# Kernel optimization log

Hardware: AMD Instinct MI355X
Metric: run time of the kernel (lower is better)

## Reference

```python
import jax, jax.numpy as jnp
import numpy as np

B, A, F = 8192, 8, 256      # batch, n_agents, per-agent obs feature dim
NA = 16                     # n_actions per agent
H1, H2 = 1024, 1024
OBS_D = A * F               # 2048 flattened obs dim
ACT_D = A * NA              # 128 joint action dim
IN_D = OBS_D + ACT_D        # 2176 MLP input dim


def setup_inputs() -> dict:
    key = jax.random.key(0)
    ks = jax.random.split(key, 8)
    s = 0.02
    return {
        "obs": jax.random.normal(ks[0], (B, A, F), dtype=jnp.float32),
        "all_actions": jax.random.uniform(ks[1], (B, ACT_D), dtype=jnp.float32),
        # per-agent stacked MLP params (agent axis first)
        "W1": jax.random.normal(ks[2], (A, IN_D, H1), dtype=jnp.float32) * s,
        "b1": jnp.zeros((A, H1), dtype=jnp.float32),
        "W2": jax.random.normal(ks[3], (A, H1, H2), dtype=jnp.float32) * s,
        "b2": jnp.zeros((A, H2), dtype=jnp.float32),
        "W3": jax.random.normal(ks[4], (A, H2, NA), dtype=jnp.float32) * s,
        "b3": jnp.zeros((A, NA), dtype=jnp.float32),
    }


def reference(obs, all_actions, W1, b1, W2, b2, W3, b3):
    b_s = obs.shape[0]
    obs_flat = obs.reshape(b_s, OBS_D)                      # [B, A*F]
    # mask[a, g] = 0 on agent a's own action block, 1 elsewhere
    mask = 1.0 - jnp.repeat(jnp.eye(A, dtype=obs.dtype), NA, axis=1)  # [A, A*NA]
    # split W1 into obs / action columns (equivalent to concat-then-dense)
    W1o = W1[:, :OBS_D, :]                                  # [A, OBS_D, H1]
    W1a = W1[:, OBS_D:, :]                                  # [A, ACT_D, H1]
    h1 = jax.nn.relu(
        jnp.einsum("bd,adh->bah", obs_flat, W1o)
        + jnp.einsum("bg,ag,agh->bah", all_actions, mask, W1a)
        + b1
    )                                                        # [B, A, H1]
    h2 = jax.nn.relu(jnp.einsum("bah,ahk->bak", h1, W2) + b2)  # [B, A, H2]
    out = jnp.einsum("bak,akn->ban", h2, W3) + b3              # [B, A, NA]
    return out.reshape(b_s, A * NA)
```

## Files before the change

### kernel.cpp

```cpp
#include <hip/hip_runtime.h>
#include <hip/hip_bf16.h>
#include <cstdint>
#include <cstddef>

typedef __bf16 bf16;
typedef __attribute__((ext_vector_type(8))) __bf16 bf16x8;
typedef __attribute__((ext_vector_type(4))) float f32x4;
typedef __attribute__((ext_vector_type(4))) int i32x4;
typedef __attribute__((address_space(3))) const bf16* lds_cp;

#define B_SZ  8192
#define NAGENT 8
#define NA_N  16
#define OBS_DD 2048
#define ACT_DD 128
#define IN_DD 2176
#define H1_D  1024
#define H2_D  1024

#define BM 256
#define BN 256
#define BK 64
#define GRID_M (B_SZ / BM)
#define GRID_N (1024 / BN)

__device__ __forceinline__ void gload16(const void* g, void* l) {
    __builtin_amdgcn_global_load_lds(
        (__attribute__((address_space(1))) void*)(g),
        (__attribute__((address_space(3))) void*)(l), 16, 0, 0);
}

__global__ void k_prep(const float* __restrict__ obs, const float* __restrict__ act,
                       bf16* __restrict__ xb, const float* __restrict__ b3,
                       float* __restrict__ out, const float* __restrict__ W3,
                       bf16* __restrict__ w3t) {
    const int NX = B_SZ * (IN_DD / 8);
    const int NO = B_SZ * 128 / 4;
    const int NW3 = NAGENT * NA_N * H2_D;
    int idx = blockIdx.x * blockDim.x + threadIdx.x;
    if (idx < NX) {
        const int chunks = IN_DD / 8;
        int b = idx / chunks;
        int c8 = idx - b * chunks;
        const float* src = (c8 < OBS_DD / 8)
            ? (obs + (size_t)b * OBS_DD + c8 * 8)
            : (act + (size_t)b * ACT_DD + (c8 - OBS_DD / 8) * 8);
        float4 v0 = ((const float4*)src)[0];
        float4 v1 = ((const float4*)src)[1];
        bf16x8 o;
        o[0] = (bf16)v0.x; o[1] = (bf16)v0.y; o[2] = (bf16)v0.z; o[3] = (bf16)v0.w;
        o[4] = (bf16)v1.x; o[5] = (bf16)v1.y; o[6] = (bf16)v1.z; o[7] = (bf16)v1.w;
        ((bf16x8*)(xb + (size_t)b * IN_DD))[c8] = o;
    } else if (idx < NX + NO) {
        int i = idx - NX;
        int c = (i & 31) * 4;
        float4 v = make_float4(b3[c], b3[c + 1], b3[c + 2], b3[c + 3]);
        ((float4*)out)[i] = v;
    } else if (idx < NX + NO + NW3) {
        int i = idx - NX - NO;
        int a = i / (NA_N * H2_D);
        int n = (i / H2_D) % NA_N;
        int k = i % H2_D;
        w3t[i] = (bf16)W3[(size_t)a * H2_D * NA_N + (size_t)k * NA_N + n];
    }
}

__global__ void k_transpose_w12(const float* __restrict__ W1, bf16* __restrict__ W1T,
                                const float* __restrict__ W2, bf16* __restrict__ W2T) {
    __shared__ float tile[32][33];
    const int z = blockIdx.z;
    const bool isW1 = (z < 8);
    const int a = isW1 ? z : z - 8;
    const int K = isW1 ? IN_DD : H1_D;
    const int H = 1024;
    const int maskStart = isW1 ? OBS_DD : (1 << 30);
    if (!isW1 && blockIdx.x >= (H1_D / 32)) return;
    const float* s = (isW1 ? W1 : W2) + (size_t)a * K * H;
    bf16* d = (isW1 ? W1T : W2T) + (size_t)a * K * H;
    int k0 = blockIdx.x * 32, h0 = blockIdx.y * 32;
    int tx = threadIdx.x, ty = threadIdx.y;
    #pragma unroll
    for (int i = 0; i < 32; i += 8) {
        int k = k0 + ty + i;
        float v = s[(size_t)k * H + h0 + tx];
        if (k >= maskStart) {
            int g = k - maskStart;
            if ((g >> 4) == a) v = 0.f;
        }
        tile[ty + i][tx] = v;
    }
    __syncthreads();
    #pragma unroll
    for (int i = 0; i < 32; i += 8) {
        d[(size_t)(h0 + ty + i) * K + k0 + tx] = (bf16)tile[tx][ty + i];
    }
}

#define DSR4(d0, d1, d2, d3, addr, O0, O1, O2, O3)                      \
    asm volatile("ds_read_b128 %0, %4 offset:" #O0 "\n\t"               \
                 "ds_read_b128 %1, %4 offset:" #O1 "\n\t"               \
                 "ds_read_b128 %2, %4 offset:" #O2 "\n\t"               \
                 "ds_read_b128 %3, %4 offset:" #O3                      \
                 : "=&v"(d0), "=&v"(d1), "=&v"(d2), "=&v"(d3)           \
                 : "v"(addr))
#define DSR2(d0, d1, addr, O0, O1)                                      \
    asm volatile("ds_read_b128 %0, %2 offset:" #O0 "\n\t"               \
                 "ds_read_b128 %1, %2 offset:" #O1                      \
                 : "=&v"(d0), "=&v"(d1) : "v"(addr))

#define BC(x) __builtin_bit_cast(bf16x8, x)

template<int FUSE>
__global__ __launch_bounds__(512, 1)
void k_gemm256(const bf16* __restrict__ Ain, size_t aStride, int lda,
               const bf16* __restrict__ Bw, const float* __restrict__ bias,
               bf16* __restrict__ Cout, size_t cStride, int K,
               int aOff, int gridZ,
               const bf16* __restrict__ W3Tp, float* __restrict__ outp) {
    extern __shared__ bf16 lds[];

    const int tid = threadIdx.x;
    const int w = tid >> 6;
    const int l = tid & 63;

    int flat = blockIdx.x + GRID_M * (blockIdx.y + GRID_N * blockIdx.z);
    int q8 = (GRID_M * GRID_N * gridZ) >> 3;
    int lin2 = (flat & 7) * q8 + (flat >> 3);
    const int ntile = lin2 % GRID_N;
    int rest = lin2 / GRID_N;
    const int mt = rest % GRID_M;
    const int az = rest / GRID_M;
    const int aw = az + aOff;

    const int rowBase = mt * BM;
    const int colBase = ntile * BN;
    const bf16* Aag = Ain + (size_t)az * aStride;
    const bf16* Bag = Bw + (size_t)aw * (size_t)1024 * K;

    const int wr = (w >> 2) * 128;
    const int wc = (w & 3) * 64;
    const int lr = l & 15;
    const int lq = l >> 4;

    const int rowA = (wr + lr) * BK;
    const int rowB = (wc + lr) * BK;
    const int ck0 = ((lq ^ (lr & 7)) * 8);
    const int ck1 = (((4 + lq) ^ (lr & 7)) * 8);

    const int sRow = w * 16 + (l >> 3);
    const int sCol = ((l & 7) ^ (l >> 3)) * 8;
    const bf16* pA0 = Aag + (size_t)(rowBase + sRow) * lda + sCol;
    const bf16* pA1 = Aag + (size_t)(rowBase + 128 + sRow) * lda + sCol;
    const bf16* pB0 = Bag + (size_t)(colBase + sRow) * K + sCol;
    const bf16* pB1 = Bag + (size_t)(colBase + 128 + sRow) * K + sCol;
    const size_t l8a = (size_t)8 * lda;
    const size_t l8b = (size_t)8 * K;

    const int nkt = K / BK;

#define STAGE_A(t1, half) do {                                              \
        const bf16* g_ = ((half) ? pA1 : pA0) + (t1) * BK;                  \
        bf16* d_ = &lds[(((t1) & 1) * 16384) + (half) * 8192 + w * 1024];   \
        gload16(g_, d_);                                                    \
        gload16(g_ + l8a, d_ + 512);                                        \
    } while (0)
#define STAGE_B(t2, half) do {                                              \
        const bf16* g_ = ((half) ? pB1 : pB0) + (t2) * BK;                  \
        bf16* d_ = &lds[32768 + (((t2) & 1) * 16384) + (half) * 8192 + w * 1024]; \
        gload16(g_, d_);                                                    \
        gload16(g_ + l8b, d_ + 512);                                        \
    } while (0)

    f32x4 acc[8][4] = {};
    i32x4 rb0, rb1, rb2, rb3, rb4, rb5, rb6, rb7;
    i32x4 pa0, pa1, pa2, pa3;
    i32x4 qa0, qa1, qa2, qa3;

#define CLUST(M0, a0, a1, a2, a3)                                           \
    do {                                                                    \
        acc[M0+0][0] = __builtin_amdgcn_mfma_f32_16x16x32_bf16(BC(a0), BC(rb0), acc[M0+0][0], 0, 0, 0); \
        acc[M0+1][0] = __builtin_amdgcn_mfma_f32_16x16x32_bf16(BC(a1), BC(rb0), acc[M0+1][0], 0, 0, 0); \
        acc[M0+0][1] = __builtin_amdgcn_mfma_f32_16x16x32_bf16(BC(a0), BC(rb1), acc[M0+0][1], 0, 0, 0); \
        acc[M0+1][1] = __builtin_amdgcn_mfma_f32_16x16x32_bf16(BC(a1), BC(rb1), acc[M0+1][1], 0, 0, 0); \
        acc[M0+0][2] = __builtin_amdgcn_mfma_f32_16x16x32_bf16(BC(a0), BC(rb2), acc[M0+0][2], 0, 0, 0); \
        acc[M0+1][2] = __builtin_amdgcn_mfma_f32_16x16x32_bf16(BC(a1), BC(rb2), acc[M0+1][2], 0, 0, 0); \
        acc[M0+0][3] = __builtin_amdgcn_mfma_f32_16x16x32_bf16(BC(a0), BC(rb3), acc[M0+0][3], 0, 0, 0); \
        acc[M0+1][3] = __builtin_amdgcn_mfma_f32_16x16x32_bf16(BC(a1), BC(rb3), acc[M0+1][3], 0, 0, 0); \
        acc[M0+0][0] = __builtin_amdgcn_mfma_f32_16x16x32_bf16(BC(a2), BC(rb4), acc[M0+0][0], 0, 0, 0); \
        acc[M0+1][0] = __builtin_amdgcn_mfma_f32_16x16x32_bf16(BC(a3), BC(rb4), acc[M0+1][0], 0, 0, 0); \
        acc[M0+0][1] = __builtin_amdgcn_mfma_f32_16x16x32_bf16(BC(a2), BC(rb5), acc[M0+0][1], 0, 0, 0); \
        acc[M0+1][1] = __builtin_amdgcn_mfma_f32_16x16x32_bf16(BC(a3), BC(rb5), acc[M0+1][1], 0, 0, 0); \
        acc[M0+0][2] = __builtin_amdgcn_mfma_f32_16x16x32_bf16(BC(a2), BC(rb6), acc[M0+0][2], 0, 0, 0); \
        acc[M0+1][2] = __builtin_amdgcn_mfma_f32_16x16x32_bf16(BC(a3), BC(rb6), acc[M0+1][2], 0, 0, 0); \
        acc[M0+0][3] = __builtin_amdgcn_mfma_f32_16x16x32_bf16(BC(a2), BC(rb7), acc[M0+0][3], 0, 0, 0); \
        acc[M0+1][3] = __builtin_amdgcn_mfma_f32_16x16x32_bf16(BC(a3), BC(rb7), acc[M0+1][3], 0, 0, 0); \
    } while (0)

    STAGE_A(0, 0); STAGE_A(0, 1);
    STAGE_B(0, 0); STAGE_B(0, 1);
    asm volatile("s_waitcnt vmcnt(0)" ::: "memory");
    __builtin_amdgcn_s_barrier();

    for (int t = 0; t < nkt; ++t) {
        const int dbuf = (t & 1) * 16384;
        lds_cp adrA0 = (lds_cp)lds + (dbuf + rowA + ck0);
        lds_cp adrA1 = (lds_cp)lds + (dbuf + rowA + ck1);
        lds_cp adrB0 = (lds_cp)lds + (32768 + dbuf + rowB + ck0);
        lds_cp adrB1 = (lds_cp)lds + (32768 + dbuf + rowB + ck1);

        DSR2(pa0, pa1, adrA0, 0, 2048);
        DSR2(pa2, pa3, adrA1, 0, 2048);
        DSR4(rb0, rb1, rb2, rb3, adrB0, 0, 2048, 4096, 6144);
        DSR4(rb4, rb5, rb6, rb7, adrB1, 0, 2048, 4096, 6144);

        if (t + 1 < nkt) {
            STAGE_A(t + 1, 0); STAGE_A(t + 1, 1);
            STAGE_B(t + 1, 0); STAGE_B(t + 1, 1);
        }

        DSR2(qa0, qa1, adrA0, 4096, 6144);
        DSR2(qa2, qa3, adrA1, 4096, 6144);

        asm volatile("s_waitcnt lgkmcnt(4)" ::: "memory");
        __builtin_amdgcn_sched_barrier(0);
        __builtin_amdgcn_s_setprio(1);
        CLUST(0, pa0, pa1, pa2, pa3);
        __builtin_amdgcn_s_setprio(0);

        DSR2(pa0, pa1, adrA0, 8192, 10240);
        DSR2(pa2, pa3, adrA1, 8192, 10240);

        asm volatile("s_waitcnt lgkmcnt(4)" ::: "memory");
        __builtin_amdgcn_sched_barrier(0);
        __builtin_amdgcn_s_setprio(1);
        CLUST(2, qa0, qa1, qa2, qa3);
        __builtin_amdgcn_s_setprio(0);

        DSR2(qa0, qa1, adrA0, 12288, 14336);
        DSR2(qa2, qa3, adrA1, 12288, 14336);

        asm volatile("s_waitcnt lgkmcnt(4)" ::: "memory");
        __builtin_amdgcn_sched_barrier(0);
        __builtin_amdgcn_s_setprio(1);
        CLUST(4, pa0, pa1, pa2, pa3);
        __builtin_amdgcn_s_setprio(0);

        asm volatile("s_waitcnt vmcnt(0)" ::: "memory");
        asm volatile("s_waitcnt lgkmcnt(0)" ::: "memory");
        __builtin_amdgcn_sched_barrier(0);
        __builtin_amdgcn_s_setprio(1);
        CLUST(6, qa0, qa1, qa2, qa3);
        __builtin_amdgcn_s_setprio(0);

        __builtin_amdgcn_s_barrier();
    }
#undef STAGE_A
#undef STAGE_B
#undef CLUST

    __syncthreads();
    const float* bAg = bias + (size_t)aw * 1024;
    float bb4[4];
    #pragma unroll
    for (int n = 0; n < 4; ++n) bb4[n] = bAg[colBase + wc + n * 16 + lr];
    #pragma unroll
    for (int m = 0; m < 8; ++m)
        #pragma unroll
        for (int n = 0; n < 4; ++n)
            #pragma unroll
            for (int r = 0; r < 4; ++r) {
                float v = acc[m][n][r] + bb4[n];
                v = fmaxf(v, 0.f);
                int row = wr + m * 16 + lq * 4 + r;
                int col = wc + n * 16 + lr;
                lds[row * 256 + ((((col >> 3) ^ (row & 7)) << 3) | (col & 7))] = (bf16)v;
            }
    __syncthreads();

    if constexpr (!FUSE) {
        bf16* Cg = Cout + (size_t)az * cStride + (size_t)rowBase * 1024 + colBase;
        const int er = tid >> 5;
        const int ec = tid & 31;
        #pragma unroll
        for (int i = 0; i < 16; ++i) {
            int row = i * 16 + er;
            int phys = ec ^ (row & 7);
            *(bf16x8*)&Cg[(size_t)row * 1024 + ec * 8] =
                *(const bf16x8*)&lds[row * 256 + phys * 8];
        }
    } else {
        const bf16* w3a = W3Tp + (size_t)aw * NA_N * H2_D;
        f32x4 oacc[2] = {};
        const int frow0 = w * 32;
        #pragma unroll
        for (int ks = 0; ks < 8; ++ks) {
            bf16x8 bfrag = *(const bf16x8*)&w3a[(size_t)lr * H2_D + colBase + ks * 32 + lq * 8];
            #pragma unroll
            for (int mm = 0; mm < 2; ++mm) {
                int row = frow0 + mm * 16 + lr;
                int lc = (ks * 4 + lq) ^ (row & 7);
                bf16x8 afrag = *(const bf16x8*)&lds[row * 256 + lc * 8];
                oacc[mm] = __builtin_amdgcn_mfma_f32_16x16x32_bf16(afrag, bfrag, oacc[mm], 0, 0, 0);
            }
        }
        #pragma unroll
        for (int mm = 0; mm < 2; ++mm)
            #pragma unroll
            for (int r = 0; r < 4; ++r)
                atomicAdd(&outp[(size_t)(rowBase + frow0 + mm * 16 + lq * 4 + r) * 128
                                + aw * NA_N + lr], oacc[mm][r]);
    }
}

extern "C" void kernel_launch(void* const* d_in, const int* in_sizes, int n_in,
                              void* d_out, int out_size, void* d_ws, size_t ws_size,
                              hipStream_t stream) {
    const float* obs = (const float*)d_in[0];
    const float* act = (const float*)d_in[1];
    const float* W1 = (const float*)d_in[2];
    const float* b1 = (const float*)d_in[3];
    const float* W2 = (const float*)d_in[4];
    const float* b2 = (const float*)d_in[5];
    const float* W3 = (const float*)d_in[6];
    const float* b3 = (const float*)d_in[7];
    float* out = (float*)d_out;

    const size_t SZ_XB  = (size_t)B_SZ * IN_DD * 2;
    const size_t SZ_W1T = (size_t)NAGENT * H1_D * IN_DD * 2;
    const size_t SZ_W2T = (size_t)NAGENT * H1_D * H2_D * 2;
    const size_t SZ_W3T = (size_t)NAGENT * NA_N * H2_D * 2;
    const size_t SZ_H1  = (size_t)B_SZ * H1_D * 2;
    const size_t SZ_FIX = SZ_XB + SZ_W1T + SZ_W2T + SZ_W3T;

    char* ws = (char*)d_ws;
    bf16* Xb  = (bf16*)ws;
    bf16* W1T = (bf16*)(ws + SZ_XB);
    bf16* W2T = (bf16*)(ws + SZ_XB + SZ_W1T);
    bf16* W3T = (bf16*)(ws + SZ_XB + SZ_W1T + SZ_W2T);
    char* hbase = ws + SZ_FIX;

    int G = 8;
    while (G > 1 && ws_size < SZ_FIX + (size_t)G * SZ_H1) G >>= 1;

    (void)hipFuncSetAttribute((const void*)k_gemm256<0>,
                              hipFuncAttributeMaxDynamicSharedMemorySize, 131072);
    (void)hipFuncSetAttribute((const void*)k_gemm256<1>,
                              hipFuncAttributeMaxDynamicSharedMemorySize, 131072);

    {
        const int NX = B_SZ * (IN_DD / 8);
        const int NO = B_SZ * 128 / 4;
        const int NW3 = NAGENT * NA_N * H2_D;
        int n = NX + NO + NW3;
        k_prep<<<(n + 255) / 256, 256, 0, stream>>>(obs, act, Xb, b3, out, W3, W3T);
    }
    k_transpose_w12<<<dim3(IN_DD / 32, 1024 / 32, 16), dim3(32, 8), 0, stream>>>(
        W1, W1T, W2, W2T);

    const size_t agElems = (size_t)B_SZ * H1_D;
    bf16* h1 = (bf16*)hbase;

    for (int g0 = 0; g0 < NAGENT; g0 += G) {
        k_gemm256<0><<<dim3(GRID_M, GRID_N, G), 512, 131072, stream>>>(
            Xb, 0, IN_DD, W1T, b1, h1, agElems, IN_DD, g0, G, nullptr, nullptr);
        k_gemm256<1><<<dim3(GRID_M, GRID_N, G), 512, 131072, stream>>>(
            h1, agElems, H1_D, W2T, b2, nullptr, 0, H1_D, g0, G, W3T, out);
    }
    (void)in_sizes; (void)n_in; (void)out_size;
}
```

Measured before the change: 418.7 us.

## Reorder MFMA k-loop into finer LDS-read/compute interleave by k-half

Restructures the inner GEMM loop so each k-half (ck0 then ck1) is processed separately, with smaller 8-MFMA clusters interleaved with finer-grained LDS reads and waitcnts. The A and B fragment loads for the second k-half are issued later, which shrinks the live register set. The global prefetch for the next tile moves to the middle of the loop. The aim is to hide LDS read latency better and lower register pressure. The trade-off is more wait points, which could expose latency if the LDS reads do not keep up.

New measurement: 407.1 us. 2.8% less time.

```diff
diff --git a/kernel.cpp b/kernel.cpp
--- a/kernel.cpp
+++ b/kernel.cpp
@@ -173,28 +173,23 @@
 
     f32x4 acc[8][4] = {};
     i32x4 rb0, rb1, rb2, rb3, rb4, rb5, rb6, rb7;
-    i32x4 pa0, pa1, pa2, pa3;
-    i32x4 qa0, qa1, qa2, qa3;
-
-#define CLUST(M0, a0, a1, a2, a3)                                           \
+    i32x4 a0, a1, a2, a3, a4, a5, a6, a7, z0, z1;
+
+#define CL8(M0, A0r, A1r, Bx0, Bx1, Bx2, Bx3)                               \
     do {                                                                    \
-        acc[M0+0][0] = __builtin_amdgcn_mfma_f32_16x16x32_bf16(BC(a0), BC(rb0), acc[M0+0][0], 0, 0, 0); \
-        acc[M0+1][0] = __builtin_amdgcn_mfma_f32_16x16x32_bf16(BC(a1), BC(rb0), acc[M0+1][0], 0, 0, 0); \
-        acc[M0+0][1] = __builtin_amdgcn_mfma_f32_16x16x32_bf16(BC(a0), BC(rb1), acc[M0+0][1], 0, 0, 0); \
-        acc[M0+1][1] = __builtin_amdgcn_mfma_f32_16x16x32_bf16(BC(a1), BC(rb1), acc[M0+1][1], 0, 0, 0); \
-        acc[M0+0][2] = __builtin_amdgcn_mfma_f32_16x16x32_bf16(BC(a0), BC(rb2), acc[M0+0][2], 0, 0, 0); \
-        acc[M0+1][2] = __builtin_amdgcn_mfma_f32_16x16x32_bf16(BC(a1), BC(rb2), acc[M0+1][2], 0, 0, 0); \
-        acc[M0+0][3] = __builtin_amdgcn_mfma_f32_16x16x32_bf16(BC(a0), BC(rb3), acc[M0+0][3], 0, 0, 0); \
-        acc[M0+1][3] = __builtin_amdgcn_mfma_f32_16x16x32_bf16(BC(a1), BC(rb3), acc[M0+1][3], 0, 0, 0); \
-        acc[M0+0][0] = __builtin_amdgcn_mfma_f32_16x16x32_bf16(BC(a2), BC(rb4), acc[M0+0][0], 0, 0, 0); \
-        acc[M0+1][0] = __builtin_amdgcn_mfma_f32_16x16x32_bf16(BC(a3), BC(rb4), acc[M0+1][0], 0, 0, 0); \
-        acc[M0+0][1] = __builtin_amdgcn_mfma_f32_16x16x32_bf16(BC(a2), BC(rb5), acc[M0+0][1], 0, 0, 0); \
-        acc[M0+1][1] = __builtin_amdgcn_mfma_f32_16x16x32_bf16(BC(a3), BC(rb5), acc[M0+1][1], 0, 0, 0); \
-        acc[M0+0][2] = __builtin_amdgcn_mfma_f32_16x16x32_bf16(BC(a2), BC(rb6), acc[M0+0][2], 0, 0, 0); \
-        acc[M0+1][2] = __builtin_amdgcn_mfma_f32_16x16x32_bf16(BC(a3), BC(rb6), acc[M0+1][2], 0, 0, 0); \
-        acc[M0+0][3] = __builtin_amdgcn_mfma_f32_16x16x32_bf16(BC(a2), BC(rb7), acc[M0+0][3], 0, 0, 0); \
-        acc[M0+1][3] = __builtin_amdgcn_mfma_f32_16x16x32_bf16(BC(a3), BC(rb7), acc[M0+1][3], 0, 0, 0); \
+        acc[M0+0][0] = __builtin_amdgcn_mfma_f32_16x16x32_bf16(BC(A0r), BC(Bx0), acc[M0+0][0], 0, 0, 0); \
+        acc[M0+1][0] = __builtin_amdgcn_mfma_f32_16x16x32_bf16(BC(A1r), BC(Bx0), acc[M0+1][0], 0, 0, 0); \
+        acc[M0+0][1] = __builtin_amdgcn_mfma_f32_16x16x32_bf16(BC(A0r), BC(Bx1), acc[M0+0][1], 0, 0, 0); \
+        acc[M0+1][1] = __builtin_amdgcn_mfma_f32_16x16x32_bf16(BC(A1r), BC(Bx1), acc[M0+1][1], 0, 0, 0); \
+        acc[M0+0][2] = __builtin_amdgcn_mfma_f32_16x16x32_bf16(BC(A0r), BC(Bx2), acc[M0+0][2], 0, 0, 0); \
+        acc[M0+1][2] = __builtin_amdgcn_mfma_f32_16x16x32_bf16(BC(A1r), BC(Bx2), acc[M0+1][2], 0, 0, 0); \
+        acc[M0+0][3] = __builtin_amdgcn_mfma_f32_16x16x32_bf16(BC(A0r), BC(Bx3), acc[M0+0][3], 0, 0, 0); \
+        acc[M0+1][3] = __builtin_amdgcn_mfma_f32_16x16x32_bf16(BC(A1r), BC(Bx3), acc[M0+1][3], 0, 0, 0); \
     } while (0)
+
+#define WAITL(N)                                                            \
+    asm volatile("s_waitcnt lgkmcnt(" #N ")" ::: "memory");                 \
+    __builtin_amdgcn_sched_barrier(0)
 
     STAGE_A(0, 0); STAGE_A(0, 1);
     STAGE_B(0, 0); STAGE_B(0, 1);
@@ -208,55 +203,68 @@
         lds_cp adrB0 = (lds_cp)lds + (32768 + dbuf + rowB + ck0);
         lds_cp adrB1 = (lds_cp)lds + (32768 + dbuf + rowB + ck1);
 
-        DSR2(pa0, pa1, adrA0, 0, 2048);
-        DSR2(pa2, pa3, adrA1, 0, 2048);
+        DSR2(a0, a1, adrA0, 0, 2048);
         DSR4(rb0, rb1, rb2, rb3, adrB0, 0, 2048, 4096, 6144);
-        DSR4(rb4, rb5, rb6, rb7, adrB1, 0, 2048, 4096, 6144);
-
+        DSR2(a2, a3, adrA0, 4096, 6144);
+
+        WAITL(2);
+        __builtin_amdgcn_s_setprio(1);
+        CL8(0, a0, a1, rb0, rb1, rb2, rb3);
+        __builtin_amdgcn_s_setprio(0);
+
+        DSR2(a4, a5, adrA0, 8192, 10240);
+        WAITL(2);
+        __builtin_amdgcn_s_setprio(1);
+        CL8(2, a2, a3, rb0, rb1, rb2, rb3);
+        __builtin_amdgcn_s_setprio(0);
+
+        DSR2(a6, a7, adrA0, 12288, 14336);
         if (t + 1 < nkt) {
             STAGE_A(t + 1, 0); STAGE_A(t + 1, 1);
             STAGE_B(t + 1, 0); STAGE_B(t + 1, 1);
         }
-
-        DSR2(qa0, qa1, adrA0, 4096, 6144);
-        DSR2(qa2, qa3, adrA1, 4096, 6144);
-
-        asm volatile("s_waitcnt lgkmcnt(4)" ::: "memory");
-        __builtin_amdgcn_sched_barrier(0);
-        __builtin_amdgcn_s_setprio(1);
-        CLUST(0, pa0, pa1, pa2, pa3);
-        __builtin_amdgcn_s_setprio(0);
-
-        DSR2(pa0, pa1, adrA0, 8192, 10240);
-        DSR2(pa2, pa3, adrA1, 8192, 10240);
-
-        asm volatile("s_waitcnt lgkmcnt(4)" ::: "memory");
-        __builtin_amdgcn_sched_barrier(0);
-        __builtin_amdgcn_s_setprio(1);
-        CLUST(2, qa0, qa1, qa2, qa3);
-        __builtin_amdgcn_s_setprio(0);
-
-        DSR2(qa0, qa1, adrA0, 12288, 14336);
-        DSR2(qa2, qa3, adrA1, 12288, 14336);
-
-        asm volatile("s_waitcnt lgkmcnt(4)" ::: "memory");
-        __builtin_amdgcn_sched_barrier(0);
-        __builtin_amdgcn_s_setprio(1);
-        CLUST(4, pa0, pa1, pa2, pa3);
+        WAITL(2);
+        __builtin_amdgcn_s_setprio(1);
+        CL8(4, a4, a5, rb0, rb1, rb2, rb3);
+        __builtin_amdgcn_s_setprio(0);
+
+        DSR2(z0, z1, adrA1, 0, 2048);
+        DSR4(rb4, rb5, rb6, rb7, adrB1, 0, 2048, 4096, 6144);
+        WAITL(6);
+        __builtin_amdgcn_s_setprio(1);
+        CL8(6, a6, a7, rb0, rb1, rb2, rb3);
+        __builtin_amdgcn_s_setprio(0);
+
+        DSR2(a0, a1, adrA1, 4096, 6144);
+        WAITL(2);
+        __builtin_amdgcn_s_setprio(1);
+        CL8(0, z0, z1, rb4, rb5, rb6, rb7);
+        __builtin_amdgcn_s_setprio(0);
+
+        DSR2(a2, a3, adrA1, 8192, 10240);
+        WAITL(2);
+        __builtin_amdgcn_s_setprio(1);
+        CL8(2, a0, a1, rb4, rb5, rb6, rb7);
+        __builtin_amdgcn_s_setprio(0);
+
+        DSR2(a4, a5, adrA1, 12288, 14336);
+        WAITL(2);
+        __builtin_amdgcn_s_setprio(1);
+        CL8(4, a2, a3, rb4, rb5, rb6, rb7);
         __builtin_amdgcn_s_setprio(0);
 
         asm volatile("s_waitcnt vmcnt(0)" ::: "memory");
-        asm volatile("s_waitcnt lgkmcnt(0)" ::: "memory");
-        __builtin_amdgcn_sched_barrier(0);
-        __builtin_amdgcn_s_setprio(1);
-        CLUST(6, qa0, qa1, qa2, qa3);
+        WAITL(0);
+        __builtin_amdgcn_s_setprio(1);
+        CL8(6, a4, a5, rb4, rb5, rb6, rb7);
         __builtin_amdgcn_s_setprio(0);
 
         __builtin_amdgcn_s_barrier();
     }
 #undef STAGE_A
 #undef STAGE_B
-#undef CLUST
+#undef CL8
+#undef WAITL
 
     __syncthreads();
     const float* bAg = bias + (size_t)aw * 1024;
```
